# Performance work log

Measured on AMD Instinct MI355X. Metric: run time of the kernel, lower is better.

Reference implementation:

```python
import jax, jax.numpy as jnp
import numpy as np
from jax import lax

GUARD_CELLS = 80
BG_CELLS = 80
ALPHA = 1.8
CFAR_UNITS = 1 + 2 * GUARD_CELLS + 2 * BG_CELLS          # 321
GUARD_UNITS = 2 * GUARD_CELLS + 1                         # 161
BG_AREA = CFAR_UNITS ** 2 - GUARD_UNITS ** 2              # background ring cell count
FRONT_DIV = (GUARD_UNITS ** 2) * ALPHA


def box_sum(x, k):
    """Same-padded KxK box sum over NCHW x (C=1), via separable 1D convs.

    Mathematically identical to a Conv2d with all-ones KxK kernel, zero bias,
    padding (k-1)//2 -- but O(N*K) instead of O(N*K^2).
    """
    p = (k - 1) // 2
    kh = jnp.ones((1, 1, k, 1), x.dtype)  # OIHW
    kw = jnp.ones((1, 1, 1, k), x.dtype)
    y = lax.conv_general_dilated(x, kh, window_strides=(1, 1), padding=[(p, p), (0, 0)])
    y = lax.conv_general_dilated(y, kw, window_strides=(1, 1), padding=[(0, 0), (p, p)])
    return y


def setup_inputs() -> dict:
    key = jax.random.key(0)
    x = jax.random.uniform(key, (4, 1, 1024, 1024), dtype=jnp.float32)
    return {"x": x}


def reference(x) -> jnp.ndarray:
    allsum = box_sum(x, CFAR_UNITS)            # conv1: 321x321 ones box
    front = box_sum(x, GUARD_UNITS)            # conv2: 161x161 ones box
    back = (allsum - front) / jnp.float32(BG_AREA)     # div1: 1x1 conv = scale
    front = front / jnp.float32(FRONT_DIV)             # div2: 1x1 conv = scale
    return front / back
```

## Files before the change

kernel.cpp:

```cpp
#include <hip/hip_runtime.h>
#include <hip/hip_bf16.h>


#define IMG 4
#define H 1024
#define W 1024
#define PADL 164
#define PADR 164
#define ROWLEN (PADL + W + PADR)

__global__ __launch_bounds__(256) void hbox_kernel(const float* __restrict__ x,
                                                   float* __restrict__ h161,
                                                   float* __restrict__ h321) {
    __shared__ float P[4][ROWLEN];
    const int wave = threadIdx.x >> 6;
    const int lane = threadIdx.x & 63;
    const int row  = (blockIdx.x << 2) + wave;

    const float4* xr = reinterpret_cast<const float4*>(x + (size_t)row * W);
    float v[16];
    {
        float4 a0 = xr[(lane << 2) + 0];
        float4 a1 = xr[(lane << 2) + 1];
        float4 a2 = xr[(lane << 2) + 2];
        float4 a3 = xr[(lane << 2) + 3];
        v[0]=a0.x; v[1]=a0.y; v[2]=a0.z; v[3]=a0.w;
        v[4]=a1.x; v[5]=a1.y; v[6]=a1.z; v[7]=a1.w;
        v[8]=a2.x; v[9]=a2.y; v[10]=a2.z; v[11]=a2.w;
        v[12]=a3.x; v[13]=a3.y; v[14]=a3.z; v[15]=a3.w;
    }
    float s = 0.f;
#pragma unroll
    for (int j = 0; j < 16; ++j) { s += v[j]; v[j] = s; }
    float t = s;
#pragma unroll
    for (int d = 1; d < 64; d <<= 1) {
        float u = __shfl_up(t, d, 64);
        if (lane >= d) t += u;
    }
    const float off = t - s;
#pragma unroll
    for (int j = 0; j < 16; ++j) v[j] += off;
    const float tot = __shfl(t, 63, 64);

    float* Pw = &P[wave][PADL];
    float4* Pr = reinterpret_cast<float4*>(Pw);
    Pr[(lane << 2) + 0] = make_float4(v[0], v[1], v[2], v[3]);
    Pr[(lane << 2) + 1] = make_float4(v[4], v[5], v[6], v[7]);
    Pr[(lane << 2) + 2] = make_float4(v[8], v[9], v[10], v[11]);
    Pr[(lane << 2) + 3] = make_float4(v[12], v[13], v[14], v[15]);
#pragma unroll
    for (int j = lane; j < PADL; j += 64) P[wave][j] = 0.f;
#pragma unroll
    for (int j = lane; j < PADR; j += 64) Pw[W + j] = tot;
    __syncthreads();

    float4* o1 = reinterpret_cast<float4*>(h161 + (size_t)row * W);
    float4* o3 = reinterpret_cast<float4*>(h321 + (size_t)row * W);
    const float* Pb = P[wave];
#pragma unroll
    for (int k = 0; k < 4; ++k) {
        const int c4 = lane + (k << 6);
        const int q  = PADL + (c4 << 2);
        const float4 hi1 = *reinterpret_cast<const float4*>(&Pb[q + 80]);
        const float4 A   = *reinterpret_cast<const float4*>(&Pb[q - 84]);
        const float4 Bv  = *reinterpret_cast<const float4*>(&Pb[q - 80]);
        const float4 hi3 = *reinterpret_cast<const float4*>(&Pb[q + 160]);
        const float4 C   = *reinterpret_cast<const float4*>(&Pb[q - 164]);
        const float4 D   = *reinterpret_cast<const float4*>(&Pb[q - 160]);
        float4 s1v, s3v;
        s1v.x = hi1.x - A.w;  s1v.y = hi1.y - Bv.x;
        s1v.z = hi1.z - Bv.y; s1v.w = hi1.w - Bv.z;
        s3v.x = hi3.x - C.w;  s3v.y = hi3.y - D.x;
        s3v.z = hi3.z - D.y;  s3v.w = hi3.w - D.z;
        o1[c4] = s1v;
        o3[c4] = s3v;
    }
}

__global__ __launch_bounds__(256) void vscan_kernel(float* __restrict__ h161,
                                                    float* __restrict__ h321,
                                                    float* __restrict__ Btot) {
    const int bx  = blockIdx.x;
    const int img = bx >> 7;
    const int b7  = bx & 127;
    const int seg = b7 >> 2;
    const int cb  = b7 & 3;
    const int col = (cb << 8) + threadIdx.x;
    const int r0  = seg << 5;

    float* p = (blockIdx.y ? h321 : h161) + ((size_t)img << 20) + col;
    float sum = 0.f;
#pragma unroll
    for (int jj = 0; jj < 32; jj += 8) {
        float a[8];
#pragma unroll
        for (int j = 0; j < 8; ++j) a[j] = p[(size_t)(r0 + jj + j) << 10];
#pragma unroll
        for (int j = 0; j < 8; ++j) { sum += a[j]; a[j] = sum; }
#pragma unroll
        for (int j = 0; j < 8; ++j) p[(size_t)(r0 + jj + j) << 10] = a[j];
    }
    Btot[((((size_t)blockIdx.y << 2) + img) << 15) + ((size_t)seg << 10) + col] = sum;
}

__global__ __launch_bounds__(256) void segscan_kernel(const float* __restrict__ Btot,
                                                      float* __restrict__ SP) {
    const int t = blockIdx.x * 256 + threadIdx.x;
    const size_t base = ((size_t)(t >> 10) << 15) + (t & 1023);
    const float* b = Btot + base;
    float* sp = SP + base;
    float off = 0.f;
#pragma unroll
    for (int s = 0; s < 32; ++s) {
        const float v = b[(size_t)s << 10];
        sp[(size_t)s << 10] = off;
        off += v;
    }
}

__global__ __launch_bounds__(256) void final_kernel(const float* __restrict__ h161,
                                                    const float* __restrict__ h321,
                                                    const float* __restrict__ SP,
                                                    float* __restrict__ out) {
    const int img = blockIdx.x >> 10;
    const int r   = blockIdx.x & 1023;
    const int c4  = threadIdx.x;

    const float4* P1 = reinterpret_cast<const float4*>(h161 + ((size_t)img << 20));
    const float4* P3 = reinterpret_cast<const float4*>(h321 + ((size_t)img << 20));
    const float4* SP1 = reinterpret_cast<const float4*>(SP) + ((size_t)img << 13);
    const float4* SP3 = SP1 + ((size_t)4 << 13);

    const int hi1 = min(r + 80, H - 1),  lo1 = r - 81;
    const int hi3 = min(r + 160, H - 1), lo3 = r - 161;

    float4 f  = P1[((size_t)hi1 << 8) + c4];
    float4 fs = SP1[(((size_t)hi1 >> 5) << 8) + c4];
    float fx = f.x + fs.x, fy = f.y + fs.y, fz = f.z + fs.z, fw = f.w + fs.w;
    if (lo1 >= 0) {
        float4 g  = P1[((size_t)lo1 << 8) + c4];
        float4 gs = SP1[(((size_t)lo1 >> 5) << 8) + c4];
        fx -= g.x + gs.x; fy -= g.y + gs.y; fz -= g.z + gs.z; fw -= g.w + gs.w;
    }
    float4 a  = P3[((size_t)hi3 << 8) + c4];
    float4 as = SP3[(((size_t)hi3 >> 5) << 8) + c4];
    float ax = a.x + as.x, ay = a.y + as.y, az = a.z + as.z, aw = a.w + as.w;
    if (lo3 >= 0) {
        float4 g  = P3[((size_t)lo3 << 8) + c4];
        float4 gs = SP3[(((size_t)lo3 >> 5) << 8) + c4];
        ax -= g.x + gs.x; ay -= g.y + gs.y; az -= g.z + gs.z; aw -= g.w + gs.w;
    }

    const float SCALE = (float)(77120.0 / 46657.8);
    float4 o;
    o.x = SCALE * fx / (ax - fx);
    o.y = SCALE * fy / (ay - fy);
    o.z = SCALE * fz / (az - fz);
    o.w = SCALE * fw / (aw - fw);
    reinterpret_cast<float4*>(out + ((size_t)img << 20) + ((size_t)r << 10))[c4] = o;
}

extern "C" void kernel_launch(void* const* d_in, const int* in_sizes, int n_in,
                              void* d_out, int out_size, void* d_ws, size_t ws_size,
                              hipStream_t stream) {
    const float* x = (const float*)d_in[0];
    float* outp = (float*)d_out;
    float* h161 = (float*)d_ws;
    float* h321 = h161 + (size_t)IMG * H * W;
    float* Btot = h321 + (size_t)IMG * H * W;
    float* SPb  = Btot + (size_t)2 * IMG * 32 * W;

    hbox_kernel<<<dim3((IMG * H) / 4), dim3(256), 0, stream>>>(x, h161, h321);
    vscan_kernel<<<dim3(512, 2), dim3(256), 0, stream>>>(h161, h321, Btot);
    segscan_kernel<<<dim3(32), dim3(256), 0, stream>>>(Btot, SPb);
    final_kernel<<<dim3(IMG * H), dim3(256), 0, stream>>>(h161, h321, SPb, outp);
}
```

Before: 96.71 us.

## Replace two horizontal box buffers with a single padded 2D prefix-sum table

Instead of writing two horizontally box-filtered images (161 and 321 wide) and scanning both vertically, the code now builds one full 2D integral image (rows padded to 1280 with the row total) and evaluates both boxes from four corners each. This halves intermediate storage and vertical-scan traffic. The cost is more gather work in the final kernel: unaligned per-element scalar loads for the left corners plus segment-prefix loads. Cancellation in large prefix sums also puts float precision at risk.

```diff
diff --git a/kernel.cpp b/kernel.cpp
--- a/kernel.cpp
+++ b/kernel.cpp
@@ -5,14 +5,12 @@
 #define IMG 4
 #define H 1024
 #define W 1024
-#define PADL 164
-#define PADR 164
-#define ROWLEN (PADL + W + PADR)
+#define WP 1280
+#define NSEG 32
+#define SEGR 32
 
-__global__ __launch_bounds__(256) void hbox_kernel(const float* __restrict__ x,
-                                                   float* __restrict__ h161,
-                                                   float* __restrict__ h321) {
-    __shared__ float P[4][ROWLEN];
+__global__ __launch_bounds__(256) void hprefix_kernel(const float* __restrict__ x,
+                                                      float* __restrict__ S) {
     const int wave = threadIdx.x >> 6;
     const int lane = threadIdx.x & 63;
     const int row  = (blockIdx.x << 2) + wave;
@@ -43,114 +41,116 @@
     for (int j = 0; j < 16; ++j) v[j] += off;
     const float tot = __shfl(t, 63, 64);
 
-    float* Pw = &P[wave][PADL];
-    float4* Pr = reinterpret_cast<float4*>(Pw);
-    Pr[(lane << 2) + 0] = make_float4(v[0], v[1], v[2], v[3]);
-    Pr[(lane << 2) + 1] = make_float4(v[4], v[5], v[6], v[7]);
-    Pr[(lane << 2) + 2] = make_float4(v[8], v[9], v[10], v[11]);
-    Pr[(lane << 2) + 3] = make_float4(v[12], v[13], v[14], v[15]);
-#pragma unroll
-    for (int j = lane; j < PADL; j += 64) P[wave][j] = 0.f;
-#pragma unroll
-    for (int j = lane; j < PADR; j += 64) Pw[W + j] = tot;
-    __syncthreads();
-
-    float4* o1 = reinterpret_cast<float4*>(h161 + (size_t)row * W);
-    float4* o3 = reinterpret_cast<float4*>(h321 + (size_t)row * W);
-    const float* Pb = P[wave];
-#pragma unroll
-    for (int k = 0; k < 4; ++k) {
-        const int c4 = lane + (k << 6);
-        const int q  = PADL + (c4 << 2);
-        const float4 hi1 = *reinterpret_cast<const float4*>(&Pb[q + 80]);
-        const float4 A   = *reinterpret_cast<const float4*>(&Pb[q - 84]);
-        const float4 Bv  = *reinterpret_cast<const float4*>(&Pb[q - 80]);
-        const float4 hi3 = *reinterpret_cast<const float4*>(&Pb[q + 160]);
-        const float4 C   = *reinterpret_cast<const float4*>(&Pb[q - 164]);
-        const float4 D   = *reinterpret_cast<const float4*>(&Pb[q - 160]);
-        float4 s1v, s3v;
-        s1v.x = hi1.x - A.w;  s1v.y = hi1.y - Bv.x;
-        s1v.z = hi1.z - Bv.y; s1v.w = hi1.w - Bv.z;
-        s3v.x = hi3.x - C.w;  s3v.y = hi3.y - D.x;
-        s3v.z = hi3.z - D.y;  s3v.w = hi3.w - D.z;
-        o1[c4] = s1v;
-        o3[c4] = s3v;
-    }
+    float4* Sr = reinterpret_cast<float4*>(S + (size_t)row * WP);
+    Sr[(lane << 2) + 0] = make_float4(v[0], v[1], v[2], v[3]);
+    Sr[(lane << 2) + 1] = make_float4(v[4], v[5], v[6], v[7]);
+    Sr[(lane << 2) + 2] = make_float4(v[8], v[9], v[10], v[11]);
+    Sr[(lane << 2) + 3] = make_float4(v[12], v[13], v[14], v[15]);
+    Sr[256 + lane]      = make_float4(tot, tot, tot, tot);
 }
 
-__global__ __launch_bounds__(256) void vscan_kernel(float* __restrict__ h161,
-                                                    float* __restrict__ h321,
+__global__ __launch_bounds__(256) void vscan_kernel(float* __restrict__ S,
                                                     float* __restrict__ Btot) {
     const int bx  = blockIdx.x;
-    const int img = bx >> 7;
-    const int b7  = bx & 127;
-    const int seg = b7 >> 2;
-    const int cb  = b7 & 3;
+    const int img = bx / 160;
+    const int rem = bx - img * 160;
+    const int seg = rem / 5;
+    const int cb  = rem - seg * 5;
     const int col = (cb << 8) + threadIdx.x;
-    const int r0  = seg << 5;
 
-    float* p = (blockIdx.y ? h321 : h161) + ((size_t)img << 20) + col;
+    float* p = S + ((size_t)img * H + (size_t)seg * SEGR) * WP + col;
     float sum = 0.f;
 #pragma unroll
-    for (int jj = 0; jj < 32; jj += 8) {
+    for (int jj = 0; jj < SEGR; jj += 8) {
         float a[8];
 #pragma unroll
-        for (int j = 0; j < 8; ++j) a[j] = p[(size_t)(r0 + jj + j) << 10];
+        for (int j = 0; j < 8; ++j) a[j] = p[(size_t)(jj + j) * WP];
 #pragma unroll
         for (int j = 0; j < 8; ++j) { sum += a[j]; a[j] = sum; }
 #pragma unroll
-        for (int j = 0; j < 8; ++j) p[(size_t)(r0 + jj + j) << 10] = a[j];
+        for (int j = 0; j < 8; ++j) p[(size_t)(jj + j) * WP] = a[j];
     }
-    Btot[((((size_t)blockIdx.y << 2) + img) << 15) + ((size_t)seg << 10) + col] = sum;
+    Btot[((size_t)img * NSEG + seg) * WP + col] = sum;
 }
 
 __global__ __launch_bounds__(256) void segscan_kernel(const float* __restrict__ Btot,
                                                       float* __restrict__ SP) {
-    const int t = blockIdx.x * 256 + threadIdx.x;
-    const size_t base = ((size_t)(t >> 10) << 15) + (t & 1023);
-    const float* b = Btot + base;
-    float* sp = SP + base;
+    const int t   = blockIdx.x * 256 + threadIdx.x;
+    const int img = t / WP;
+    const int col = t - img * WP;
+    const float* b = Btot + (size_t)img * NSEG * WP + col;
+    float*     sp = SP   + (size_t)img * NSEG * WP + col;
     float off = 0.f;
 #pragma unroll
-    for (int s = 0; s < 32; ++s) {
-        const float v = b[(size_t)s << 10];
-        sp[(size_t)s << 10] = off;
+    for (int sg = 0; sg < NSEG; ++sg) {
+        const float v = b[(size_t)sg * WP];
+        sp[(size_t)sg * WP] = off;
         off += v;
     }
 }
 
-__global__ __launch_bounds__(256) void final_kernel(const float* __restrict__ h161,
-                                                    const float* __restrict__ h321,
+__global__ __launch_bounds__(256) void final_kernel(const float* __restrict__ S,
                                                     const float* __restrict__ SP,
                                                     float* __restrict__ out) {
     const int img = blockIdx.x >> 10;
     const int r   = blockIdx.x & 1023;
     const int c4  = threadIdx.x;
+    const int cb  = c4 << 2;
 
-    const float4* P1 = reinterpret_cast<const float4*>(h161 + ((size_t)img << 20));
-    const float4* P3 = reinterpret_cast<const float4*>(h321 + ((size_t)img << 20));
-    const float4* SP1 = reinterpret_cast<const float4*>(SP) + ((size_t)img << 13);
-    const float4* SP3 = SP1 + ((size_t)4 << 13);
+    const float* Si  = S  + (size_t)img * H * WP;
+    const float* SPi = SP + (size_t)img * NSEG * WP;
 
-    const int hi1 = min(r + 80, H - 1),  lo1 = r - 81;
-    const int hi3 = min(r + 160, H - 1), lo3 = r - 161;
+    const int R3h = min(r + 160, H - 1), R3l = r - 161;
+    const int R1h = min(r + 80,  H - 1), R1l = r - 81;
+    const int CH3 = cb + 160, CH1 = cb + 80;
 
-    float4 f  = P1[((size_t)hi1 << 8) + c4];
-    float4 fs = SP1[(((size_t)hi1 >> 5) << 8) + c4];
-    float fx = f.x + fs.x, fy = f.y + fs.y, fz = f.z + fs.z, fw = f.w + fs.w;
-    if (lo1 >= 0) {
-        float4 g  = P1[((size_t)lo1 << 8) + c4];
-        float4 gs = SP1[(((size_t)lo1 >> 5) << 8) + c4];
-        fx -= g.x + gs.x; fy -= g.y + gs.y; fz -= g.z + gs.z; fw -= g.w + gs.w;
+#define P4(row, c) ({                                                          \
+        const float4 _a = *reinterpret_cast<const float4*>(Si + (size_t)(row) * WP + (c));   \
+        const float4 _b = *reinterpret_cast<const float4*>(SPi + (size_t)((row) >> 5) * WP + (c)); \
+        make_float4(_a.x + _b.x, _a.y + _b.y, _a.z + _b.z, _a.w + _b.w); })
+
+    float ax, ay, az, aw, fx, fy, fz, fw;
+    {
+        const float4 A = P4(R3h, CH3);
+        float lo[4];
+#pragma unroll
+        for (int i = 0; i < 4; ++i) {
+            const int c = cb + i - 161;
+            lo[i] = (c >= 0) ? (Si[(size_t)R3h * WP + c] + SPi[(size_t)(R3h >> 5) * WP + c]) : 0.f;
+        }
+        ax = A.x - lo[0]; ay = A.y - lo[1]; az = A.z - lo[2]; aw = A.w - lo[3];
     }
-    float4 a  = P3[((size_t)hi3 << 8) + c4];
-    float4 as = SP3[(((size_t)hi3 >> 5) << 8) + c4];
-    float ax = a.x + as.x, ay = a.y + as.y, az = a.z + as.z, aw = a.w + as.w;
-    if (lo3 >= 0) {
-        float4 g  = P3[((size_t)lo3 << 8) + c4];
-        float4 gs = SP3[(((size_t)lo3 >> 5) << 8) + c4];
-        ax -= g.x + gs.x; ay -= g.y + gs.y; az -= g.z + gs.z; aw -= g.w + gs.w;
+    if (R3l >= 0) {
+        const float4 B = P4(R3l, CH3);
+        float lo[4];
+#pragma unroll
+        for (int i = 0; i < 4; ++i) {
+            const int c = cb + i - 161;
+            lo[i] = (c >= 0) ? (Si[(size_t)R3l * WP + c] + SPi[(size_t)(R3l >> 5) * WP + c]) : 0.f;
+        }
+        ax -= B.x - lo[0]; ay -= B.y - lo[1]; az -= B.z - lo[2]; aw -= B.w - lo[3];
     }
+    {
+        const float4 Fq = P4(R1h, CH1);
+        float lo[4];
+#pragma unroll
+        for (int i = 0; i < 4; ++i) {
+            const int c = cb + i - 81;
+            lo[i] = (c >= 0) ? (Si[(size_t)R1h * WP + c] + SPi[(size_t)(R1h >> 5) * WP + c]) : 0.f;
+        }
+        fx = Fq.x - lo[0]; fy = Fq.y - lo[1]; fz = Fq.z - lo[2]; fw = Fq.w - lo[3];
+    }
+    if (R1l >= 0) {
+        const float4 G = P4(R1l, CH1);
+        float lo[4];
+#pragma unroll
+        for (int i = 0; i < 4; ++i) {
+            const int c = cb + i - 81;
+            lo[i] = (c >= 0) ? (Si[(size_t)R1l * WP + c] + SPi[(size_t)(R1l >> 5) * WP + c]) : 0.f;
+        }
+        fx -= G.x - lo[0]; fy -= G.y - lo[1]; fz -= G.z - lo[2]; fw -= G.w - lo[3];
+    }
+#undef P4
 
     const float SCALE = (float)(77120.0 / 46657.8);
     float4 o;
@@ -166,13 +166,12 @@
                               hipStream_t stream) {
     const float* x = (const float*)d_in[0];
     float* outp = (float*)d_out;
-    float* h161 = (float*)d_ws;
-    float* h321 = h161 + (size_t)IMG * H * W;
-    float* Btot = h321 + (size_t)IMG * H * W;
-    float* SPb  = Btot + (size_t)2 * IMG * 32 * W;
+    float* S    = (float*)d_ws;
+    float* Btot = S + (size_t)IMG * H * WP;
+    float* SPb  = Btot + (size_t)IMG * NSEG * WP;
 
-    hbox_kernel<<<dim3((IMG * H) / 4), dim3(256), 0, stream>>>(x, h161, h321);
-    vscan_kernel<<<dim3(512, 2), dim3(256), 0, stream>>>(h161, h321, Btot);
-    segscan_kernel<<<dim3(32), dim3(256), 0, stream>>>(Btot, SPb);
-    final_kernel<<<dim3(IMG * H), dim3(256), 0, stream>>>(h161, h321, SPb, outp);
+    hprefix_kernel<<<dim3((IMG * H) / 4), dim3(256), 0, stream>>>(x, S);
+    vscan_kernel<<<dim3(IMG * NSEG * 5), dim3(256), 0, stream>>>(S, Btot);
+    segscan_kernel<<<dim3(20), dim3(256), 0, stream>>>(Btot, SPb);
+    final_kernel<<<dim3(IMG * H), dim3(256), 0, stream>>>(S, SPb, outp);
 }
```

Measured after the change: 116.5 us. +20.4%, slower.

## Fuse horizontal box and vertical segment scan into one kernel

Applied to the files above, without the earlier changes.

Merges the horizontal box-sum kernel and the vertical in-segment scan into one kernel. Each block processes an 8-row segment in shared memory and writes vertically accumulated prefix rows plus segment totals directly. This removes the read-modify-write pass over both 16MB intermediates and one kernel launch. In exchange, the segment-totals scan now runs sequentially over 128 segments with only 32 blocks, which lengthens that serial kernel, and the fused kernel uses twice the shared memory per block.

```diff
diff --git a/kernel.cpp b/kernel.cpp
--- a/kernel.cpp
+++ b/kernel.cpp
@@ -5,150 +5,145 @@
 #define IMG 4
 #define H 1024
 #define W 1024
+#define SEGR 8
+#define NSEG 128
 #define PADL 164
 #define PADR 164
 #define ROWLEN (PADL + W + PADR)
 
-__global__ __launch_bounds__(256) void hbox_kernel(const float* __restrict__ x,
-                                                   float* __restrict__ h161,
-                                                   float* __restrict__ h321) {
-    __shared__ float P[4][ROWLEN];
+__global__ __launch_bounds__(256) void hseg_kernel(const float* __restrict__ x,
+                                                   float* __restrict__ g161,
+                                                   float* __restrict__ g321,
+                                                   float* __restrict__ Btot) {
+    __shared__ float P[SEGR][ROWLEN];
     const int wave = threadIdx.x >> 6;
     const int lane = threadIdx.x & 63;
-    const int row  = (blockIdx.x << 2) + wave;
+    const int img  = blockIdx.x >> 7;
+    const int seg  = blockIdx.x & 127;
+    const int r0   = seg << 3;
 
-    const float4* xr = reinterpret_cast<const float4*>(x + (size_t)row * W);
-    float v[16];
     {
-        float4 a0 = xr[(lane << 2) + 0];
-        float4 a1 = xr[(lane << 2) + 1];
-        float4 a2 = xr[(lane << 2) + 2];
-        float4 a3 = xr[(lane << 2) + 3];
-        v[0]=a0.x; v[1]=a0.y; v[2]=a0.z; v[3]=a0.w;
-        v[4]=a1.x; v[5]=a1.y; v[6]=a1.z; v[7]=a1.w;
-        v[8]=a2.x; v[9]=a2.y; v[10]=a2.z; v[11]=a2.w;
-        v[12]=a3.x; v[13]=a3.y; v[14]=a3.z; v[15]=a3.w;
+        const int j0 = wave << 1;
+        const float4* xr0 = reinterpret_cast<const float4*>(
+            x + (((size_t)img << 10) + r0 + j0) * W);
+        const float4* xr1 = reinterpret_cast<const float4*>(
+            x + (((size_t)img << 10) + r0 + j0 + 1) * W);
+        float4 a[2][4];
+#pragma unroll
+        for (int q = 0; q < 4; ++q) a[0][q] = xr0[(lane << 2) + q];
+#pragma unroll
+        for (int q = 0; q < 4; ++q) a[1][q] = xr1[(lane << 2) + q];
+
+#pragma unroll
+        for (int rr = 0; rr < 2; ++rr) {
+            float v[16];
+            v[0]=a[rr][0].x; v[1]=a[rr][0].y; v[2]=a[rr][0].z; v[3]=a[rr][0].w;
+            v[4]=a[rr][1].x; v[5]=a[rr][1].y; v[6]=a[rr][1].z; v[7]=a[rr][1].w;
+            v[8]=a[rr][2].x; v[9]=a[rr][2].y; v[10]=a[rr][2].z; v[11]=a[rr][2].w;
+            v[12]=a[rr][3].x; v[13]=a[rr][3].y; v[14]=a[rr][3].z; v[15]=a[rr][3].w;
+            float s = 0.f;
+#pragma unroll
+            for (int j = 0; j < 16; ++j) { s += v[j]; v[j] = s; }
+            float t = s;
+#pragma unroll
+            for (int d = 1; d < 64; d <<= 1) {
+                float u = __shfl_up(t, d, 64);
+                if (lane >= d) t += u;
+            }
+            const float off = t - s;
+#pragma unroll
+            for (int j = 0; j < 16; ++j) v[j] += off;
+            const float tot = __shfl(t, 63, 64);
+
+            float* row = P[j0 + rr];
+            float4* Pr = reinterpret_cast<float4*>(row + PADL);
+            Pr[(lane << 2) + 0] = make_float4(v[0], v[1], v[2], v[3]);
+            Pr[(lane << 2) + 1] = make_float4(v[4], v[5], v[6], v[7]);
+            Pr[(lane << 2) + 2] = make_float4(v[8], v[9], v[10], v[11]);
+            Pr[(lane << 2) + 3] = make_float4(v[12], v[13], v[14], v[15]);
+            float4* Pz = reinterpret_cast<float4*>(row);
+            if (lane < 41) {
+                Pz[lane]       = make_float4(0.f, 0.f, 0.f, 0.f);
+                Pz[297 + lane] = make_float4(tot, tot, tot, tot);
+            }
+        }
     }
-    float s = 0.f;
-#pragma unroll
-    for (int j = 0; j < 16; ++j) { s += v[j]; v[j] = s; }
-    float t = s;
-#pragma unroll
-    for (int d = 1; d < 64; d <<= 1) {
-        float u = __shfl_up(t, d, 64);
-        if (lane >= d) t += u;
-    }
-    const float off = t - s;
-#pragma unroll
-    for (int j = 0; j < 16; ++j) v[j] += off;
-    const float tot = __shfl(t, 63, 64);
-
-    float* Pw = &P[wave][PADL];
-    float4* Pr = reinterpret_cast<float4*>(Pw);
-    Pr[(lane << 2) + 0] = make_float4(v[0], v[1], v[2], v[3]);
-    Pr[(lane << 2) + 1] = make_float4(v[4], v[5], v[6], v[7]);
-    Pr[(lane << 2) + 2] = make_float4(v[8], v[9], v[10], v[11]);
-    Pr[(lane << 2) + 3] = make_float4(v[12], v[13], v[14], v[15]);
-#pragma unroll
-    for (int j = lane; j < PADL; j += 64) P[wave][j] = 0.f;
-#pragma unroll
-    for (int j = lane; j < PADR; j += 64) Pw[W + j] = tot;
     __syncthreads();
 
-    float4* o1 = reinterpret_cast<float4*>(h161 + (size_t)row * W);
-    float4* o3 = reinterpret_cast<float4*>(h321 + (size_t)row * W);
-    const float* Pb = P[wave];
+    const int c4 = threadIdx.x;
+    const int q  = PADL + (c4 << 2);
+    float s1x=0.f,s1y=0.f,s1z=0.f,s1w=0.f;
+    float s3x=0.f,s3y=0.f,s3z=0.f,s3w=0.f;
+    float4* o1 = reinterpret_cast<float4*>(g161 + (((size_t)img << 10) + r0) * W) + c4;
+    float4* o3 = reinterpret_cast<float4*>(g321 + (((size_t)img << 10) + r0) * W) + c4;
+
 #pragma unroll
-    for (int k = 0; k < 4; ++k) {
-        const int c4 = lane + (k << 6);
-        const int q  = PADL + (c4 << 2);
+    for (int j = 0; j < SEGR; ++j) {
+        const float* Pb = P[j];
         const float4 hi1 = *reinterpret_cast<const float4*>(&Pb[q + 80]);
         const float4 A   = *reinterpret_cast<const float4*>(&Pb[q - 84]);
         const float4 Bv  = *reinterpret_cast<const float4*>(&Pb[q - 80]);
         const float4 hi3 = *reinterpret_cast<const float4*>(&Pb[q + 160]);
         const float4 C   = *reinterpret_cast<const float4*>(&Pb[q - 164]);
         const float4 D   = *reinterpret_cast<const float4*>(&Pb[q - 160]);
-        float4 s1v, s3v;
-        s1v.x = hi1.x - A.w;  s1v.y = hi1.y - Bv.x;
-        s1v.z = hi1.z - Bv.y; s1v.w = hi1.w - Bv.z;
-        s3v.x = hi3.x - C.w;  s3v.y = hi3.y - D.x;
-        s3v.z = hi3.z - D.y;  s3v.w = hi3.w - D.z;
-        o1[c4] = s1v;
-        o3[c4] = s3v;
+        s1x += hi1.x - A.w;  s1y += hi1.y - Bv.x;
+        s1z += hi1.z - Bv.y; s1w += hi1.w - Bv.z;
+        s3x += hi3.x - C.w;  s3y += hi3.y - D.x;
+        s3z += hi3.z - D.y;  s3w += hi3.w - D.z;
+        o1[(size_t)j << 8] = make_float4(s1x, s1y, s1z, s1w);
+        o3[(size_t)j << 8] = make_float4(s3x, s3y, s3z, s3w);
     }
-}
-
-__global__ __launch_bounds__(256) void vscan_kernel(float* __restrict__ h161,
-                                                    float* __restrict__ h321,
-                                                    float* __restrict__ Btot) {
-    const int bx  = blockIdx.x;
-    const int img = bx >> 7;
-    const int b7  = bx & 127;
-    const int seg = b7 >> 2;
-    const int cb  = b7 & 3;
-    const int col = (cb << 8) + threadIdx.x;
-    const int r0  = seg << 5;
-
-    float* p = (blockIdx.y ? h321 : h161) + ((size_t)img << 20) + col;
-    float sum = 0.f;
-#pragma unroll
-    for (int jj = 0; jj < 32; jj += 8) {
-        float a[8];
-#pragma unroll
-        for (int j = 0; j < 8; ++j) a[j] = p[(size_t)(r0 + jj + j) << 10];
-#pragma unroll
-        for (int j = 0; j < 8; ++j) { sum += a[j]; a[j] = sum; }
-#pragma unroll
-        for (int j = 0; j < 8; ++j) p[(size_t)(r0 + jj + j) << 10] = a[j];
-    }
-    Btot[((((size_t)blockIdx.y << 2) + img) << 15) + ((size_t)seg << 10) + col] = sum;
+    float4* b1 = reinterpret_cast<float4*>(Btot + ((size_t)img * NSEG + seg) * W);
+    float4* b3 = reinterpret_cast<float4*>(Btot + ((size_t)(IMG + img) * NSEG + seg) * W);
+    b1[c4] = make_float4(s1x, s1y, s1z, s1w);
+    b3[c4] = make_float4(s3x, s3y, s3z, s3w);
 }
 
 __global__ __launch_bounds__(256) void segscan_kernel(const float* __restrict__ Btot,
                                                       float* __restrict__ SP) {
     const int t = blockIdx.x * 256 + threadIdx.x;
-    const size_t base = ((size_t)(t >> 10) << 15) + (t & 1023);
+    const size_t base = ((size_t)(t >> 10) * NSEG) * W + (t & 1023);
     const float* b = Btot + base;
     float* sp = SP + base;
     float off = 0.f;
-#pragma unroll
-    for (int s = 0; s < 32; ++s) {
-        const float v = b[(size_t)s << 10];
-        sp[(size_t)s << 10] = off;
+#pragma unroll 8
+    for (int sg = 0; sg < NSEG; ++sg) {
+        const float v = b[(size_t)sg << 10];
+        sp[(size_t)sg << 10] = off;
         off += v;
     }
 }
 
-__global__ __launch_bounds__(256) void final_kernel(const float* __restrict__ h161,
-                                                    const float* __restrict__ h321,
+__global__ __launch_bounds__(256) void final_kernel(const float* __restrict__ g161,
+                                                    const float* __restrict__ g321,
                                                     const float* __restrict__ SP,
                                                     float* __restrict__ out) {
     const int img = blockIdx.x >> 10;
     const int r   = blockIdx.x & 1023;
     const int c4  = threadIdx.x;
 
-    const float4* P1 = reinterpret_cast<const float4*>(h161 + ((size_t)img << 20));
-    const float4* P3 = reinterpret_cast<const float4*>(h321 + ((size_t)img << 20));
-    const float4* SP1 = reinterpret_cast<const float4*>(SP) + ((size_t)img << 13);
-    const float4* SP3 = SP1 + ((size_t)4 << 13);
+    const float4* P1 = reinterpret_cast<const float4*>(g161 + ((size_t)img << 20));
+    const float4* P3 = reinterpret_cast<const float4*>(g321 + ((size_t)img << 20));
+    const float4* SP1 = reinterpret_cast<const float4*>(SP) + ((size_t)img << 15);
+    const float4* SP3 = reinterpret_cast<const float4*>(SP) + ((size_t)(IMG + img) << 15);
 
     const int hi1 = min(r + 80, H - 1),  lo1 = r - 81;
     const int hi3 = min(r + 160, H - 1), lo3 = r - 161;
 
     float4 f  = P1[((size_t)hi1 << 8) + c4];
-    float4 fs = SP1[(((size_t)hi1 >> 5) << 8) + c4];
+    float4 fs = SP1[(((size_t)hi1 >> 3) << 8) + c4];
     float fx = f.x + fs.x, fy = f.y + fs.y, fz = f.z + fs.z, fw = f.w + fs.w;
     if (lo1 >= 0) {
         float4 g  = P1[((size_t)lo1 << 8) + c4];
-        float4 gs = SP1[(((size_t)lo1 >> 5) << 8) + c4];
+        float4 gs = SP1[(((size_t)lo1 >> 3) << 8) + c4];
         fx -= g.x + gs.x; fy -= g.y + gs.y; fz -= g.z + gs.z; fw -= g.w + gs.w;
     }
     float4 a  = P3[((size_t)hi3 << 8) + c4];
-    float4 as = SP3[(((size_t)hi3 >> 5) << 8) + c4];
+    float4 as = SP3[(((size_t)hi3 >> 3) << 8) + c4];
     float ax = a.x + as.x, ay = a.y + as.y, az = a.z + as.z, aw = a.w + as.w;
     if (lo3 >= 0) {
         float4 g  = P3[((size_t)lo3 << 8) + c4];
-        float4 gs = SP3[(((size_t)lo3 >> 5) << 8) + c4];
+        float4 gs = SP3[(((size_t)lo3 >> 3) << 8) + c4];
         ax -= g.x + gs.x; ay -= g.y + gs.y; az -= g.z + gs.z; aw -= g.w + gs.w;
     }
 
@@ -166,13 +161,12 @@
                               hipStream_t stream) {
     const float* x = (const float*)d_in[0];
     float* outp = (float*)d_out;
-    float* h161 = (float*)d_ws;
-    float* h321 = h161 + (size_t)IMG * H * W;
-    float* Btot = h321 + (size_t)IMG * H * W;
-    float* SPb  = Btot + (size_t)2 * IMG * 32 * W;
+    float* g161 = (float*)d_ws;
+    float* g321 = g161 + (size_t)IMG * H * W;
+    float* Btot = g321 + (size_t)IMG * H * W;
+    float* SPb  = Btot + (size_t)2 * IMG * NSEG * W;
 
-    hbox_kernel<<<dim3((IMG * H) / 4), dim3(256), 0, stream>>>(x, h161, h321);
-    vscan_kernel<<<dim3(512, 2), dim3(256), 0, stream>>>(h161, h321, Btot);
+    hseg_kernel<<<dim3(IMG * NSEG), dim3(256), 0, stream>>>(x, g161, g321, Btot);
     segscan_kernel<<<dim3(32), dim3(256), 0, stream>>>(Btot, SPb);
-    final_kernel<<<dim3(IMG * H), dim3(256), 0, stream>>>(h161, h321, SPb, outp);
+    final_kernel<<<dim3(IMG * H), dim3(256), 0, stream>>>(g161, g321, SPb, outp);
 }
```

After: 100.0 us. 1.03x slower.
